# Performance work log

Measured on AMD Instinct MI355X. Metric: run time of the kernel, lower is better.

Reference implementation:

```python
import jax, jax.numpy as jnp
import numpy as np

DIM = 1024
DEPTH = 3
BATCH = 8
SEQ = DIM  # module requires seq_len == dim for the residual add to broadcast


def setup_inputs() -> dict:
    key = jax.random.key(0)
    k1, k2, k3, k4 = jax.random.split(key, 4)
    x = jax.random.normal(k1, (BATCH, SEQ, DIM), dtype=jnp.float32)
    # torch.nn.Linear(dim, 3*dim): weight [3*dim, dim], bias [3*dim]
    Wqkv = jax.random.normal(k2, (3 * DIM, DIM), dtype=jnp.float32) * (1.0 / np.sqrt(DIM))
    bqkv = jax.random.normal(k3, (3 * DIM,), dtype=jnp.float32) * 0.01
    # self.w: Parameter of shape [depth, dim, dim], init randn
    w = jax.random.normal(k4, (DEPTH, DIM, DIM), dtype=jnp.float32)
    return {"x": x, "Wqkv": Wqkv, "bqkv": bqkv, "w": w}


def reference(x, Wqkv, bqkv, w):
    # qkv projection then chunk into q, k, v along last dim
    qkv = x @ Wqkv.T + bqkv                      # [B, S, 3*dim]
    q, k, v = jnp.split(qkv, 3, axis=-1)         # each [B, S, dim]
    scale = 1.0 / (q.shape[-1] ** 0.5)
    # sum over depth of (q @ w[i]) @ k^T, accumulated onto v
    # einsum contracts d (dim), e (dim), and sums over n (depth) in one pass
    scores = jnp.einsum('bsd,nde,bte->bst', q, w, k)  # [B, S, S]; requires S == dim
    return v + scores * scale
```

## Files before the change

kernel.cpp:

```cpp
#include <hip/hip_runtime.h>
#include <hip/hip_bf16.h>
#include <stdint.h>

typedef __bf16 bf16_t;
typedef __bf16 bf16x8 __attribute__((ext_vector_type(8)));
typedef __bf16 bf16x4 __attribute__((ext_vector_type(4)));
typedef float  f32x4  __attribute__((ext_vector_type(4)));

#define DIM   1024
#define BATCH 8
#define SCALE 0.03125f


__device__ __forceinline__ float rowdot_bf16(const bf16_t* __restrict__ row,
                                             const float* __restrict__ vec, int lane) {
    float s = 0.f;
#pragma unroll
    for (int c = 0; c < 2; ++c) {
        const int d0 = (lane + c * 64) * 8;
        const bf16x8 v = *reinterpret_cast<const bf16x8*>(row + d0);
#pragma unroll
        for (int e = 0; e < 8; ++e) s += vec[d0 + e] * (float)v[e];
    }
#pragma unroll
    for (int off = 32; off; off >>= 1) s += __shfl_down(s, off);
    return s;
}

__device__ __forceinline__ void gemm_sk(const bf16_t* __restrict__ A, const bf16_t* __restrict__ B,
                                        float* __restrict__ oP, int s, int tid,
                                        bf16_t* As, bf16_t* Bs)
{
    const int wave = tid >> 6, lane = tid & 63;
    const int bm = (s >> 5) * 128;
    const int bn = ((s >> 2) & 7) * 128;
    const int kb = (s & 3) * 256;
    float* outP  = oP + (long)(s & 3) * 1048576;
    const int wr = wave >> 1, wc = wave & 1;
    const int lhi = lane >> 4, llo = lane & 15;

    f32x4 acc[4][4];
    const f32x4 fz = {0.f, 0.f, 0.f, 0.f};
#pragma unroll
    for (int i = 0; i < 4; ++i)
#pragma unroll
        for (int j = 0; j < 4; ++j) acc[i][j] = fz;

    for (int k0 = 0; k0 < 256; k0 += 32) {
#pragma unroll
        for (int i = 0; i < 2; ++i) {
            const int c  = wave * 128 + i * 64 + lane;
            const int r  = c >> 2;
            const int cc = (c & 3) << 3;
            const long ga = (long)(bm + r) * 1024 + kb + k0 + cc;
            const long gb = (long)(bn + r) * 1024 + kb + k0 + cc;
            const int lbase = (wave * 128 + i * 64) << 3;
            __builtin_amdgcn_global_load_lds(
                (const __attribute__((address_space(1))) uint32_t*)(A + ga),
                (__attribute__((address_space(3))) uint32_t*)(&As[lbase]), 16, 0, 0);
            __builtin_amdgcn_global_load_lds(
                (const __attribute__((address_space(1))) uint32_t*)(B + gb),
                (__attribute__((address_space(3))) uint32_t*)(&Bs[lbase]), 16, 0, 0);
        }
        __syncthreads();

        bf16x8 af[4], bfr[4];
#pragma unroll
        for (int mi = 0; mi < 4; ++mi)
            af[mi] = *reinterpret_cast<const bf16x8*>(&As[(wr * 64 + mi * 16 + llo) * 32 + lhi * 8]);
#pragma unroll
        for (int ni = 0; ni < 4; ++ni)
            bfr[ni] = *reinterpret_cast<const bf16x8*>(&Bs[(wc * 64 + ni * 16 + llo) * 32 + lhi * 8]);
#pragma unroll
        for (int mi = 0; mi < 4; ++mi)
#pragma unroll
            for (int ni = 0; ni < 4; ++ni)
                acc[mi][ni] = __builtin_amdgcn_mfma_f32_16x16x32_bf16(af[mi], bfr[ni], acc[mi][ni], 0, 0, 0);
        __syncthreads();
    }

#pragma unroll
    for (int mi = 0; mi < 4; ++mi) {
        const int r0 = bm + wr * 64 + mi * 16 + lhi * 4;
#pragma unroll
        for (int ni = 0; ni < 4; ++ni) {
            const int cg = bn + wc * 64 + ni * 16 + llo;
            const f32x4 v = acc[mi][ni];
#pragma unroll
            for (int j = 0; j < 4; ++j)
                outP[(long)(r0 + j) * 1024 + cg] = v[j];
        }
    }
}

__global__ __launch_bounds__(256)
void k_prep(const float* __restrict__ x, const float* __restrict__ Wqkv,
            const float* __restrict__ w,
            bf16_t* __restrict__ xb, bf16_t* __restrict__ wvb,
            bf16_t* __restrict__ weff, bf16_t* __restrict__ wtb,
            bf16_t* __restrict__ wqt, bf16_t* __restrict__ wkt)
{
    __shared__ float tile[32][33];
    const int b = blockIdx.x;
    if (b < 8192) {
        const int i = b * 256 + threadIdx.x;
        const float4 v = reinterpret_cast<const float4*>(x)[i];
        bf16x4 o;
        o.x = (bf16_t)v.x; o.y = (bf16_t)v.y; o.z = (bf16_t)v.z; o.w = (bf16_t)v.w;
        reinterpret_cast<bf16x4*>(xb)[i] = o;
    } else if (b < 9216) {
        const int i = (b - 8192) * 256 + threadIdx.x;
        const float4 v = reinterpret_cast<const float4*>(Wqkv + 2097152)[i];
        bf16x4 o;
        o.x = (bf16_t)v.x; o.y = (bf16_t)v.y; o.z = (bf16_t)v.z; o.w = (bf16_t)v.w;
        reinterpret_cast<bf16x4*>(wvb)[i] = o;
    } else if (b < 10240) {
        const int t  = b - 9216;
        const int tx = threadIdx.x & 31, ty = threadIdx.x >> 5;
        const int d0 = (t & 31) * 32, e0 = (t >> 5) * 32;
#pragma unroll
        for (int r = 0; r < 4; ++r) {
            const int d = d0 + r * 8 + ty;
            const int e = e0 + tx;
            const float sum =
                w[d * 1024 + e] + w[1048576 + d * 1024 + e] + w[2097152 + d * 1024 + e];
            tile[r * 8 + ty][tx] = sum;
            weff[(long)d * 1024 + e] = (bf16_t)sum;
        }
        __syncthreads();
#pragma unroll
        for (int r = 0; r < 4; ++r) {
            const int e = e0 + r * 8 + ty;
            const int d = d0 + tx;
            wtb[(long)e * 1024 + d] = (bf16_t)tile[tx][r * 8 + ty];
        }
    } else {
        const bool isQ = (b < 11264);
        const int t  = b - (isQ ? 10240 : 11264);
        const float* src = isQ ? Wqkv : (Wqkv + 1048576);
        bf16_t* dst = isQ ? wqt : wkt;
        const int tx = threadIdx.x & 31, ty = threadIdx.x >> 5;
        const int e0 = (t & 31) * 32, d0 = (t >> 5) * 32;
#pragma unroll
        for (int r = 0; r < 4; ++r)
            tile[r * 8 + ty][tx] = src[(long)(e0 + r * 8 + ty) * 1024 + d0 + tx];
        __syncthreads();
#pragma unroll
        for (int r = 0; r < 4; ++r)
            dst[(long)(d0 + r * 8 + ty) * 1024 + e0 + tx] = (bf16_t)tile[tx][r * 8 + ty];
    }
}

__global__ __launch_bounds__(256)
void k_midA(const bf16_t* __restrict__ wkt, const bf16_t* __restrict__ weff,
            const bf16_t* __restrict__ wtb, const float* __restrict__ bqkv,
            float* __restrict__ pX1, float* __restrict__ h1, float* __restrict__ h2)
{
    __shared__ __align__(16) bf16_t As[128 * 32];
    __shared__ __align__(16) bf16_t Bs[128 * 32];
    if (blockIdx.x < 256) {
        gemm_sk(wkt, weff, pX1, blockIdx.x, threadIdx.x, As, Bs);
        return;
    }
    const int wave = threadIdx.x >> 6, lane = threadIdx.x & 63;
    const int r = ((int)blockIdx.x - 256) * 4 + wave;
    if (r < 1024) {
        const float s = rowdot_bf16(weff + (long)r * 1024, bqkv + 1024, lane);
        if (lane == 0) h1[r] = s;
    } else {
        const float s = rowdot_bf16(wtb + (long)(r - 1024) * 1024, bqkv, lane);
        if (lane == 0) h2[r - 1024] = s;
    }
}

__global__ __launch_bounds__(256)
void k_cvtA(const float* __restrict__ p, bf16_t* __restrict__ X1b,
            const bf16_t* __restrict__ wqt, const bf16_t* __restrict__ wkt,
            const float* __restrict__ h1, const float* __restrict__ h2,
            const float* __restrict__ bqkv,
            float* __restrict__ u, float* __restrict__ w2, float* __restrict__ cO)
{
    const int b = blockIdx.x;
    if (b < 1024) {
        const int i = b * 256 + threadIdx.x;
        const f32x4* rp = reinterpret_cast<const f32x4*>(p);
        const f32x4 a0 = rp[i], a1 = rp[i + 262144], a2 = rp[i + 524288], a3 = rp[i + 786432];
        bf16x4 o;
        o.x = (bf16_t)(a0.x + a1.x + a2.x + a3.x);
        o.y = (bf16_t)(a0.y + a1.y + a2.y + a3.y);
        o.z = (bf16_t)(a0.z + a1.z + a2.z + a3.z);
        o.w = (bf16_t)(a0.w + a1.w + a2.w + a3.w);
        reinterpret_cast<bf16x4*>(X1b)[i] = o;
    } else if (b < 1536) {
        const int wave = threadIdx.x >> 6, lane = threadIdx.x & 63;
        const int rr = (b - 1024) * 4 + wave;
        if (rr < 1024) {
            const float s = rowdot_bf16(wqt + (long)rr * 1024, h1, lane);
            if (lane == 0) u[rr] = s;
        } else {
            const float s = rowdot_bf16(wkt + (long)(rr - 1024) * 1024, h2, lane);
            if (lane == 0) w2[rr - 1024] = s;
        }
    } else {
        if (threadIdx.x < 64) {
            float s = 0.f;
            for (int i = threadIdx.x; i < 1024; i += 64) s += bqkv[i] * h1[i];
#pragma unroll
            for (int off = 32; off; off >>= 1) s += __shfl_down(s, off);
            if (threadIdx.x == 0) cO[0] = s;
        }
    }
}

__global__ __launch_bounds__(256)
void k_midB(const bf16_t* __restrict__ X1b, const bf16_t* __restrict__ wqt,
            float* __restrict__ pMT, const bf16_t* __restrict__ xb,
            const float* __restrict__ u, const float* __restrict__ w2,
            const float* __restrict__ cO,
            float* __restrict__ RU, float* __restrict__ RW)
{
    __shared__ __align__(16) bf16_t As[128 * 32];
    __shared__ __align__(16) bf16_t Bs[128 * 32];
    if (blockIdx.x < 256) {
        gemm_sk(X1b, wqt, pMT, blockIdx.x, threadIdx.x, As, Bs);
        return;
    }
    const int wave = threadIdx.x >> 6, lane = threadIdx.x & 63;
    const int s = ((int)blockIdx.x - 256) * 4 + wave;
    const bf16_t* row = xb + (long)s * 1024;
    float s1 = 0.f, s2 = 0.f;
#pragma unroll
    for (int c = 0; c < 2; ++c) {
        const int d0 = (lane + c * 64) * 8;
        const bf16x8 v = *reinterpret_cast<const bf16x8*>(row + d0);
#pragma unroll
        for (int e = 0; e < 8; ++e) {
            const float f = (float)v[e];
            s1 += u[d0 + e] * f;
            s2 += w2[d0 + e] * f;
        }
    }
#pragma unroll
    for (int off = 32; off; off >>= 1) { s1 += __shfl_down(s1, off); s2 += __shfl_down(s2, off); }
    if (lane == 0) {
        RU[s] = SCALE * (s1 + cO[0]);
        RW[s] = SCALE * s2;
    }
}

__global__ __launch_bounds__(256)
void k_cvtS(const float* __restrict__ p, bf16_t* __restrict__ out) {
    const int i = blockIdx.x * 256 + threadIdx.x;
    const f32x4* rp = reinterpret_cast<const f32x4*>(p);
    const f32x4 a0 = rp[i], a1 = rp[i + 262144], a2 = rp[i + 524288], a3 = rp[i + 786432];
    bf16x4 o;
    o.x = (bf16_t)(SCALE * (a0.x + a1.x + a2.x + a3.x));
    o.y = (bf16_t)(SCALE * (a0.y + a1.y + a2.y + a3.y));
    o.z = (bf16_t)(SCALE * (a0.z + a1.z + a2.z + a3.z));
    o.w = (bf16_t)(SCALE * (a0.w + a1.w + a2.w + a3.w));
    reinterpret_cast<bf16x4*>(out)[i] = o;
}

#define GLOAD(SRC, DST) __builtin_amdgcn_global_load_lds( \
    (const __attribute__((address_space(1))) uint32_t*)(SRC), \
    (__attribute__((address_space(3))) uint32_t*)(DST), 16, 0, 0)

template<int MODE>
__global__ __launch_bounds__(512, 2)
void k_db2(const bf16_t* __restrict__ A1, const bf16_t* __restrict__ A2,
           const bf16_t* __restrict__ B1, const bf16_t* __restrict__ B2,
           const float* __restrict__ RUv, const float* __restrict__ RWv,
           const float* __restrict__ bv,
           bf16_t* __restrict__ oT, float* __restrict__ oF)
{
    constexpr int SLOT = 32768;
    constexpr int NTT  = (MODE == 0) ? 16 : 32;
    __shared__ __align__(16) unsigned char slds[2 * SLOT];

    const int tid  = threadIdx.x;
    const int wave = tid >> 6, lane = tid & 63;
    const int wm = wave >> 2, wn = wave & 3;
    const int llo = lane & 15, lhi = lane >> 4;

    int bm, bn, z = 0;
    const int nw = ((int)blockIdx.x & 7) * 64 + ((int)blockIdx.x >> 3);
    if (MODE == 0) {
        bm = (nw >> 3) * 128;
        bn = (nw & 7) * 128;
    } else {
        z = nw >> 6;
        const int r = nw & 63;
        bm = (r >> 3) * 128; bn = (r & 7) * 128;
    }
    const long zo = (long)z << 20;

    const bf16_t *sA1[2], *sB1[2], *sA2[2], *sB2[2];
    int dA[2], dB[2];
#pragma unroll
    for (int j = 0; j < 2; ++j) {
        const int C = j * 512 + tid;
        const int r = C >> 3, u = (C & 7) ^ (r & 7);
        const long aoff = (long)(bm + r) * 1024 + (u << 3);
        const long boff = (long)(bn + r) * 1024 + (u << 3);
        sA1[j] = A1 + zo + aoff;  dA[j] = C << 4;
        sB1[j] = B1 + zo + boff;  dB[j] = 16384 + (C << 4);
        if (MODE == 1) { sA2[j] = A2 + zo + aoff; sB2[j] = B2 + boff; }
    }

    auto stage = [&](int tt) {
        unsigned char* s = &slds[(tt & 1) * SLOT];
        const long ko = (long)(tt & 15) << 6;
        const bool hB = (MODE == 1) && (tt >= 16);
#pragma unroll
        for (int j = 0; j < 2; ++j) {
            GLOAD((hB ? sA2[j] : sA1[j]) + ko, s + dA[j]);
            GLOAD((hB ? sB2[j] : sB1[j]) + ko, s + dB[j]);
        }
    };

    f32x4 acc[4][2];
    const f32x4 fz = {0.f, 0.f, 0.f, 0.f};
#pragma unroll
    for (int i = 0; i < 4; ++i)
#pragma unroll
        for (int j = 0; j < 2; ++j) acc[i][j] = fz;

    stage(0);

    for (int t = 0; t < NTT; ++t) {
        if (t + 1 < NTT) {
            stage(t + 1);
            asm volatile("s_waitcnt vmcnt(4)" ::: "memory");
        } else {
            asm volatile("s_waitcnt vmcnt(0)" ::: "memory");
        }
        __builtin_amdgcn_s_barrier();

        const unsigned char* sb = &slds[(t & 1) * SLOT];
#pragma unroll
        for (int ks = 0; ks < 2; ++ks) {
            bf16x8 af[4], bfv[2];
#pragma unroll
            for (int mi = 0; mi < 4; ++mi) {
                const int r = wm * 64 + mi * 16 + llo;
                af[mi] = *reinterpret_cast<const bf16x8*>(
                    sb + r * 128 + ((((ks << 2) | lhi) ^ (r & 7)) << 4));
            }
#pragma unroll
            for (int ni = 0; ni < 2; ++ni) {
                const int r = wn * 32 + ni * 16 + llo;
                bfv[ni] = *reinterpret_cast<const bf16x8*>(
                    sb + 16384 + r * 128 + ((((ks << 2) | lhi) ^ (r & 7)) << 4));
            }
            __builtin_amdgcn_s_setprio(1);
#pragma unroll
            for (int mi = 0; mi < 4; ++mi)
#pragma unroll
                for (int ni = 0; ni < 2; ++ni)
                    acc[mi][ni] = __builtin_amdgcn_mfma_f32_16x16x32_bf16(
                        af[mi], bfv[ni], acc[mi][ni], 0, 0, 0);
            __builtin_amdgcn_s_setprio(0);
        }
        asm volatile("s_waitcnt lgkmcnt(0)" ::: "memory");
        __builtin_amdgcn_s_barrier();
    }

#pragma unroll
    for (int mi = 0; mi < 4; ++mi) {
        const int lr0 = bm + wm * 64 + mi * 16 + lhi * 4;
#pragma unroll
        for (int ni = 0; ni < 2; ++ni) {
            const int cg = bn + wn * 32 + ni * 16 + llo;
            const f32x4 v = acc[mi][ni];
            if (MODE == 0) {
#pragma unroll
                for (int j = 0; j < 4; ++j)
                    oT[(long)(lr0 + j) * 1024 + cg] = (bf16_t)v[j];
            } else {
                const float cterm = RWv[z * 1024 + cg] + bv[cg];
#pragma unroll
                for (int j = 0; j < 4; ++j) {
                    const int lr = lr0 + j;
                    oF[zo + (long)lr * 1024 + cg] = v[j] + RUv[z * 1024 + lr] + cterm;
                }
            }
        }
    }
}
#undef GLOAD

extern "C" void kernel_launch(void* const* d_in, const int* in_sizes, int n_in,
                              void* d_out, int out_size, void* d_ws, size_t ws_size,
                              hipStream_t stream) {
    const float* x    = (const float*)d_in[0];
    const float* Wqkv = (const float*)d_in[1];
    const float* bqkv = (const float*)d_in[2];
    const float* w    = (const float*)d_in[3];
    float* out = (float*)d_out;

    char* ws = (char*)d_ws;
    bf16_t* xb   = (bf16_t*)ws;
    float*  pbig = (float*) (ws + (16l << 20));
    bf16_t* tsb  = (bf16_t*)(ws + (16l << 20));
    bf16_t* weff = (bf16_t*)(ws + (32l << 20));
    bf16_t* wtb  = (bf16_t*)(ws + (34l << 20));
    bf16_t* wqt  = (bf16_t*)(ws + (36l << 20));
    bf16_t* wkt  = (bf16_t*)(ws + (38l << 20));
    bf16_t* wvb  = (bf16_t*)(ws + (40l << 20));
    bf16_t* X1b  = (bf16_t*)(ws + (42l << 20));
    bf16_t* MTb  = (bf16_t*)(ws + (44l << 20));
    char*   sm   = ws + (46l << 20);
    float* h1 = (float*)sm;
    float* h2 = (float*)(sm + 4096);
    float* u  = (float*)(sm + 8192);
    float* w2 = (float*)(sm + 12288);
    float* cO = (float*)(sm + 16384);
    float* RU = (float*)(sm + 20480);
    float* RW = (float*)(sm + 53248);
    if (ws_size < (size_t)(54l << 20) + 65536) return;

    k_prep<<<12288, 256, 0, stream>>>(x, Wqkv, w, xb, wvb, weff, wtb, wqt, wkt);

    k_midA<<<768, 256, 0, stream>>>(wkt, weff, wtb, bqkv, pbig, h1, h2);

    k_cvtA<<<1537, 256, 0, stream>>>(pbig, X1b, wqt, wkt, h1, h2, bqkv, u, w2, cO);

    k_midB<<<2304, 256, 0, stream>>>(X1b, wqt, pbig, xb, u, w2, cO, RU, RW);

    k_cvtS<<<1024, 256, 0, stream>>>(pbig, MTb);

    k_db2<0><<<512, 512, 0, stream>>>(xb, nullptr, MTb, nullptr,
                                      nullptr, nullptr, nullptr, tsb, nullptr);

    k_db2<1><<<512, 512, 0, stream>>>(tsb, xb, xb, wvb,
                                      RU, RW, bqkv + 2048, nullptr, out);
}
```

Measured before the change: 108.1 us.

## Switch final GEMMs to 32x32x16 MFMA with 4-wave blocks and new swizzle

Replaces the 16x16x32 MFMA tiling of the two final GEMM kernels with 32x32x16 MFMAs. Each block now has 4 waves instead of 8, and each wave computes a 64x64 sub-tile instead of 64x32. The LDS swizzle now also mixes in row bits 3-4, to avoid bank conflicts with the wider fragment reads. The aim is fewer LDS fragment reads per FLOP and denser MFMA issue, at the cost of more accumulator registers per thread and fewer waves to hide latency.

```diff
diff --git a/kernel.cpp b/kernel.cpp
--- a/kernel.cpp
+++ b/kernel.cpp
@@ -6,6 +6,7 @@
 typedef __bf16 bf16x8 __attribute__((ext_vector_type(8)));
 typedef __bf16 bf16x4 __attribute__((ext_vector_type(4)));
 typedef float  f32x4  __attribute__((ext_vector_type(4)));
+typedef float  f32x16 __attribute__((ext_vector_type(16)));
 
 #define DIM   1024
 #define BATCH 8
@@ -265,13 +266,15 @@
     (const __attribute__((address_space(1))) uint32_t*)(SRC), \
     (__attribute__((address_space(3))) uint32_t*)(DST), 16, 0, 0)
 
+__device__ __forceinline__ int fswz(int r) { return (r & 7) ^ ((r >> 3) & 3); }
+
 template<int MODE>
-__global__ __launch_bounds__(512, 2)
-void k_db2(const bf16_t* __restrict__ A1, const bf16_t* __restrict__ A2,
-           const bf16_t* __restrict__ B1, const bf16_t* __restrict__ B2,
-           const float* __restrict__ RUv, const float* __restrict__ RWv,
-           const float* __restrict__ bv,
-           bf16_t* __restrict__ oT, float* __restrict__ oF)
+__global__ __launch_bounds__(256, 2)
+void k_mm32(const bf16_t* __restrict__ A1, const bf16_t* __restrict__ A2,
+            const bf16_t* __restrict__ B1, const bf16_t* __restrict__ B2,
+            const float* __restrict__ RUv, const float* __restrict__ RWv,
+            const float* __restrict__ bv,
+            bf16_t* __restrict__ oT, float* __restrict__ oF)
 {
     constexpr int SLOT = 32768;
     constexpr int NTT  = (MODE == 0) ? 16 : 32;
@@ -279,8 +282,8 @@
 
     const int tid  = threadIdx.x;
     const int wave = tid >> 6, lane = tid & 63;
-    const int wm = wave >> 2, wn = wave & 3;
-    const int llo = lane & 15, lhi = lane >> 4;
+    const int wmm = wave >> 1, wnn = wave & 1;
+    const int lr = lane & 31, lk = lane >> 5;
 
     int bm, bn, z = 0;
     const int nw = ((int)blockIdx.x & 7) * 64 + ((int)blockIdx.x >> 3);
@@ -294,17 +297,23 @@
     }
     const long zo = (long)z << 20;
 
-    const bf16_t *sA1[2], *sB1[2], *sA2[2], *sB2[2];
-    int dA[2], dB[2];
-#pragma unroll
-    for (int j = 0; j < 2; ++j) {
-        const int C = j * 512 + tid;
-        const int r = C >> 3, u = (C & 7) ^ (r & 7);
-        const long aoff = (long)(bm + r) * 1024 + (u << 3);
-        const long boff = (long)(bn + r) * 1024 + (u << 3);
-        sA1[j] = A1 + zo + aoff;  dA[j] = C << 4;
-        sB1[j] = B1 + zo + boff;  dB[j] = 16384 + (C << 4);
-        if (MODE == 1) { sA2[j] = A2 + zo + aoff; sB2[j] = B2 + boff; }
+    const bf16_t *s1[8], *s2[8]; int dst[8];
+#pragma unroll
+    for (int j = 0; j < 8; ++j) {
+        const int C = (j & 3) * 256 + tid;
+        const int r = C >> 3;
+        const int u = (C & 7) ^ fswz(r);
+        if (j < 4) {
+            const long off = (long)(bm + r) * 1024 + (u << 3);
+            s1[j] = A1 + zo + off;
+            s2[j] = (MODE == 1) ? (A2 + zo + off) : nullptr;
+            dst[j] = C << 4;
+        } else {
+            const long off = (long)(bn + r) * 1024 + (u << 3);
+            s1[j] = B1 + ((MODE == 1) ? zo : 0) + off;
+            s2[j] = (MODE == 1) ? (B2 + off) : nullptr;
+            dst[j] = 16384 + (C << 4);
+        }
     }
 
     auto stage = [&](int tt) {
@@ -312,76 +321,81 @@
         const long ko = (long)(tt & 15) << 6;
         const bool hB = (MODE == 1) && (tt >= 16);
 #pragma unroll
-        for (int j = 0; j < 2; ++j) {
-            GLOAD((hB ? sA2[j] : sA1[j]) + ko, s + dA[j]);
-            GLOAD((hB ? sB2[j] : sB1[j]) + ko, s + dB[j]);
-        }
+        for (int j = 0; j < 8; ++j)
+            GLOAD((hB ? s2[j] : s1[j]) + ko, s + dst[j]);
     };
 
-    f32x4 acc[4][2];
-    const f32x4 fz = {0.f, 0.f, 0.f, 0.f};
-#pragma unroll
-    for (int i = 0; i < 4; ++i)
-#pragma unroll
-        for (int j = 0; j < 2; ++j) acc[i][j] = fz;
+    f32x16 acc[2][2];
+#pragma unroll
+    for (int i = 0; i < 2; ++i)
+#pragma unroll
+        for (int j = 0; j < 2; ++j)
+#pragma unroll
+            for (int q = 0; q < 16; ++q) acc[i][j][q] = 0.f;
 
     stage(0);
 
     for (int t = 0; t < NTT; ++t) {
         if (t + 1 < NTT) {
             stage(t + 1);
-            asm volatile("s_waitcnt vmcnt(4)" ::: "memory");
+            asm volatile("s_waitcnt vmcnt(8)" ::: "memory");
         } else {
             asm volatile("s_waitcnt vmcnt(0)" ::: "memory");
         }
         __builtin_amdgcn_s_barrier();
 
         const unsigned char* sb = &slds[(t & 1) * SLOT];
-#pragma unroll
-        for (int ks = 0; ks < 2; ++ks) {
-            bf16x8 af[4], bfv[2];
-#pragma unroll
-            for (int mi = 0; mi < 4; ++mi) {
-                const int r = wm * 64 + mi * 16 + llo;
-                af[mi] = *reinterpret_cast<const bf16x8*>(
-                    sb + r * 128 + ((((ks << 2) | lhi) ^ (r & 7)) << 4));
-            }
-#pragma unroll
-            for (int ni = 0; ni < 2; ++ni) {
-                const int r = wn * 32 + ni * 16 + llo;
-                bfv[ni] = *reinterpret_cast<const bf16x8*>(
-                    sb + 16384 + r * 128 + ((((ks << 2) | lhi) ^ (r & 7)) << 4));
-            }
-            __builtin_amdgcn_s_setprio(1);
-#pragma unroll
-            for (int mi = 0; mi < 4; ++mi)
-#pragma unroll
-                for (int ni = 0; ni < 2; ++ni)
-                    acc[mi][ni] = __builtin_amdgcn_mfma_f32_16x16x32_bf16(
-                        af[mi], bfv[ni], acc[mi][ni], 0, 0, 0);
-            __builtin_amdgcn_s_setprio(0);
-        }
+        bf16x8 af[2][4], bf[2][4];
+#pragma unroll
+        for (int mb = 0; mb < 2; ++mb) {
+            const int r = wmm * 64 + mb * 32 + lr;
+            const int f = fswz(r);
+#pragma unroll
+            for (int s = 0; s < 4; ++s)
+                af[mb][s] = *reinterpret_cast<const bf16x8*>(
+                    sb + r * 128 + ((((s << 1) | lk) ^ f) << 4));
+        }
+#pragma unroll
+        for (int nb = 0; nb < 2; ++nb) {
+            const int r = wnn * 64 + nb * 32 + lr;
+            const int f = fswz(r);
+#pragma unroll
+            for (int s = 0; s < 4; ++s)
+                bf[nb][s] = *reinterpret_cast<const bf16x8*>(
+                    sb + 16384 + r * 128 + ((((s << 1) | lk) ^ f) << 4));
+        }
+        __builtin_amdgcn_s_setprio(1);
+#pragma unroll
+        for (int s = 0; s < 4; ++s)
+#pragma unroll
+            for (int mb = 0; mb < 2; ++mb)
+#pragma unroll
+                for (int nb = 0; nb < 2; ++nb)
+                    acc[mb][nb] = __builtin_amdgcn_mfma_f32_32x32x16_bf16(
+                        af[mb][s], bf[nb][s], acc[mb][nb], 0, 0, 0);
+        __builtin_amdgcn_s_setprio(0);
         asm volatile("s_waitcnt lgkmcnt(0)" ::: "memory");
         __builtin_amdgcn_s_barrier();
     }
 
 #pragma unroll
-    for (int mi = 0; mi < 4; ++mi) {
-        const int lr0 = bm + wm * 64 + mi * 16 + lhi * 4;
-#pragma unroll
-        for (int ni = 0; ni < 2; ++ni) {
-            const int cg = bn + wn * 32 + ni * 16 + llo;
-            const f32x4 v = acc[mi][ni];
-            if (MODE == 0) {
-#pragma unroll
-                for (int j = 0; j < 4; ++j)
-                    oT[(long)(lr0 + j) * 1024 + cg] = (bf16_t)v[j];
-            } else {
-                const float cterm = RWv[z * 1024 + cg] + bv[cg];
-#pragma unroll
-                for (int j = 0; j < 4; ++j) {
-                    const int lr = lr0 + j;
-                    oF[zo + (long)lr * 1024 + cg] = v[j] + RUv[z * 1024 + lr] + cterm;
+    for (int mb = 0; mb < 2; ++mb) {
+#pragma unroll
+        for (int nb = 0; nb < 2; ++nb) {
+            const int cg = bn + wnn * 64 + nb * 32 + lr;
+            const float cterm = (MODE == 1) ? (RWv[z * 1024 + cg] + bv[cg]) : 0.f;
+#pragma unroll
+            for (int g = 0; g < 4; ++g) {
+                const int r0 = bm + wmm * 64 + mb * 32 + g * 8 + lk * 4;
+#pragma unroll
+                for (int q = 0; q < 4; ++q) {
+                    const float val = acc[mb][nb][g * 4 + q];
+                    if (MODE == 0) {
+                        oT[(long)(r0 + q) * 1024 + cg] = (bf16_t)val;
+                    } else {
+                        oF[zo + (long)(r0 + q) * 1024 + cg] =
+                            val + RUv[z * 1024 + r0 + q] + cterm;
+                    }
                 }
             }
         }
@@ -429,9 +443,9 @@
 
     k_cvtS<<<1024, 256, 0, stream>>>(pbig, MTb);
 
-    k_db2<0><<<512, 512, 0, stream>>>(xb, nullptr, MTb, nullptr,
-                                      nullptr, nullptr, nullptr, tsb, nullptr);
-
-    k_db2<1><<<512, 512, 0, stream>>>(tsb, xb, xb, wvb,
-                                      RU, RW, bqkv + 2048, nullptr, out);
-}
+    k_mm32<0><<<512, 256, 0, stream>>>(xb, nullptr, MTb, nullptr,
+                                       nullptr, nullptr, nullptr, tsb, nullptr);
+
+    k_mm32<1><<<512, 256, 0, stream>>>(tsb, xb, xb, wvb,
+                                       RU, RW, bqkv + 2048, nullptr, out);
+}
```

After: 113.9 us. 5.4% more time.
